# Kernel tuning notes

Measured on AMD Instinct MI355X. Metric: run time of the kernel, lower is better.

Reference implementation:

```python
import jax, jax.numpy as jnp
import numpy as np

D_MODEL = 1024
N_HEADS = 16
D_HEAD = D_MODEL // N_HEADS
WINDOW = 64
SCALE = 1.0 / np.sqrt(D_HEAD)


def setup_inputs() -> dict:
    key = jax.random.key(0)
    k1, k2, k3 = jax.random.split(key, 3)
    B, N = 1, 4096
    x = jax.random.normal(k1, (B, N, D_MODEL), dtype=jnp.float32)
    # xavier-uniform-ish init for weights (scaled normal is fine for a numeric reference)
    w_qkv = jax.random.normal(k2, (3 * D_MODEL, D_MODEL), dtype=jnp.float32) * (1.0 / np.sqrt(D_MODEL))
    b_qkv = jnp.zeros((3 * D_MODEL,), dtype=jnp.float32)
    w_out = jax.random.normal(k3, (D_MODEL, D_MODEL), dtype=jnp.float32) * (1.0 / np.sqrt(D_MODEL))
    b_out = jnp.zeros((D_MODEL,), dtype=jnp.float32)
    return {"x": x, "w_qkv": w_qkv, "b_qkv": b_qkv, "w_out": w_out, "b_out": b_out}


def reference(x, w_qkv, b_qkv, w_out, b_out):
    B, N, D = x.shape
    # QKV projection (torch Linear: x @ W^T + b)
    qkv = x @ w_qkv.T + b_qkv                      # [B, N, 3D]
    qkv = qkv.reshape(B, N, 3, N_HEADS, D_HEAD)
    qkv = jnp.transpose(qkv, (2, 0, 3, 1, 4))       # [3, B, H, N, dh]
    q, k, v = qkv[0], qkv[1], qkv[2]
    # dense scores, masked to causal sliding window (faithful to original)
    scores = jnp.einsum('bhqd,bhkd->bhqk', q, k) * SCALE  # [B, H, N, N]
    qpos = jnp.arange(N)[:, None]
    kpos = jnp.arange(N)[None, :]
    diff = qpos - kpos
    mask = (diff >= 0) & (diff < WINDOW)            # [N, N]
    scores = jnp.where(mask[None, None, :, :], scores, -jnp.inf)
    attn = jax.nn.softmax(scores, axis=-1)          # every query has >=1 valid key (self)
    out = jnp.einsum('bhqk,bhkd->bhqd', attn, v)    # [B, H, N, dh]
    out = jnp.transpose(out, (0, 2, 1, 3)).reshape(B, N, D)
    out = out @ w_out.T + b_out
    return out
```

## Files before the change

kernel.cpp:

```cpp
#include <hip/hip_runtime.h>
#include <hip/hip_bf16.h>
#include <stdint.h>
#include <stddef.h>

#define NSEQ  4096
#define DM    1024
#define NHEAD 16
#define DHEAD 64
#define WIN   64

using short8 = __attribute__((ext_vector_type(8))) short;
using f32x4  = __attribute__((ext_vector_type(4))) float;

#define GLOBAL_AS __attribute__((address_space(1)))
#define LDS_AS    __attribute__((address_space(3)))

__device__ __forceinline__ unsigned short f2bf(float f) {
  union { float f; unsigned int u; } v; v.f = f;
  unsigned int r = v.u + 0x7FFFu + ((v.u >> 16) & 1u);
  return (unsigned short)(r >> 16);
}

__device__ __forceinline__ void gload_lds16(void* lds, const void* g) {
  __builtin_amdgcn_global_load_lds((const GLOBAL_AS unsigned int*)g,
                                   (LDS_AS unsigned int*)lds, 16, 0, 0);
}

#define NX4 1048576
#define NW4 786432
__global__ void cvt_all(const float* __restrict__ x,
                        const float* __restrict__ wqkv,
                        const float* __restrict__ wout,
                        unsigned short* __restrict__ dst) {
  int i = blockIdx.x * blockDim.x + threadIdx.x;
  float4 f;
  if (i < NX4)            f = ((const float4*)x)[i];
  else if (i < NX4 + NW4) f = ((const float4*)wqkv)[i - NX4];
  else                    f = ((const float4*)wout)[i - (NX4 + NW4)];
  ushort4 o;
  o.x = f2bf(f.x); o.y = f2bf(f.y); o.z = f2bf(f.z); o.w = f2bf(f.w);
  ((ushort4*)dst)[i] = o;
}

template<int EPI>
__global__ __launch_bounds__(256)
void gemm3(const unsigned short* __restrict__ A,
           const unsigned short* __restrict__ B,
           const float* __restrict__ bias,
           float* __restrict__ Cf,
           unsigned short* __restrict__ qo,
           unsigned short* __restrict__ ko,
           unsigned short* __restrict__ vo,
           int M, int N, int K) {
  __shared__ short lds[3][8192];

  const int nbn = N >> 7;
  const int bm  = blockIdx.x / nbn;
  const int bn  = blockIdx.x % nbn;
  const int m0  = bm << 7, n0 = bn << 7;
  const int tid = threadIdx.x, w = tid >> 6, l = tid & 63;
  const int wr  = w >> 1, wc = w & 1;
  const int l15 = l & 15, l4 = l >> 4;

  const int skel = ((l & 3) << 3) ^ ((l >= 32) << 4);
  const int roff = l15 * 32 + ((l4 * 8) ^ ((l15 >= 8) * 16));

  f32x4 acc[4][4] = {};
  const int NT = K >> 5;

  auto stage = [&](int t) {
    const int buf = t % 3;
    const int kb  = t << 5;
#pragma unroll
    for (int r = 0; r < 2; ++r) {
      const int c   = r * 4 + w;
      const int row = c * 16 + (l >> 2);
      gload_lds16(&lds[buf][c * 512 + l * 8],
                  A + (size_t)(m0 + row) * K + kb + skel);
      gload_lds16(&lds[buf][4096 + c * 512 + l * 8],
                  B + (size_t)(n0 + row) * K + kb + skel);
    }
  };

  stage(0);
  stage(1);
  asm volatile("s_waitcnt vmcnt(4)" ::: "memory");
  __builtin_amdgcn_s_barrier();

  for (int t = 0; t < NT; ++t) {
    const short* Ab = &lds[t % 3][0];
    const short* Bb = &lds[t % 3][4096];
    short8 af[4], bf[4];
#pragma unroll
    for (int i = 0; i < 4; ++i) {
      af[i] = *(const short8*)&Ab[(wr * 4 + i) * 512 + roff];
      bf[i] = *(const short8*)&Bb[(wc * 4 + i) * 512 + roff];
    }
    if (t + 2 < NT) stage(t + 2);
    if (t + 2 < NT)       asm volatile("s_waitcnt vmcnt(4)" ::: "memory");
    else if (t + 2 == NT) asm volatile("s_waitcnt vmcnt(0)" ::: "memory");
    __builtin_amdgcn_s_barrier();
    __builtin_amdgcn_s_setprio(1);
#pragma unroll
    for (int mi = 0; mi < 4; ++mi)
#pragma unroll
      for (int ni = 0; ni < 4; ++ni)
        acc[mi][ni] = __builtin_amdgcn_mfma_f32_16x16x32_bf16(
            af[mi], bf[ni], acc[mi][ni], 0, 0, 0);
    __builtin_amdgcn_s_setprio(0);
  }

  if (EPI == 0) {
#pragma unroll
    for (int ni = 0; ni < 4; ++ni) {
      const int n  = n0 + wc * 64 + ni * 16 + l15;
      const float bv = bias[n];
      const int region = n >> 10;
#pragma unroll
      for (int mi = 0; mi < 4; ++mi) {
        const int mb = m0 + wr * 64 + mi * 16 + l4 * 4;
        if (region == 0) {
          const int h = (n >> 6) & 15, d = n & 63;
#pragma unroll
          for (int r = 0; r < 4; ++r)
            qo[((size_t)(h * NSEQ + mb + r)) * DHEAD + d] =
                f2bf((acc[mi][ni][r] + bv) * 0.125f);
        } else if (region == 1) {
          const int nn = n - 1024;
          const int h = nn >> 6, d = nn & 63;
#pragma unroll
          for (int r = 0; r < 4; ++r)
            ko[((size_t)(h * NSEQ + mb + r)) * DHEAD + d] =
                f2bf(acc[mi][ni][r] + bv);
        } else {
          const int nn = n - 2048;
          ushort4 pk;
          pk.x = f2bf(acc[mi][ni][0] + bv);
          pk.y = f2bf(acc[mi][ni][1] + bv);
          pk.z = f2bf(acc[mi][ni][2] + bv);
          pk.w = f2bf(acc[mi][ni][3] + bv);
          *(ushort4*)&vo[(size_t)nn * NSEQ + mb] = pk;
        }
      }
    }
  } else {
#pragma unroll
    for (int ni = 0; ni < 4; ++ni) {
      const int n  = n0 + wc * 64 + ni * 16 + l15;
      const float bv = bias[n];
#pragma unroll
      for (int mi = 0; mi < 4; ++mi) {
        const int mb = m0 + wr * 64 + mi * 16 + l4 * 4;
#pragma unroll
        for (int r = 0; r < 4; ++r)
          Cf[(size_t)(mb + r) * N + n] = acc[mi][ni][r] + bv;
      }
    }
  }
}

__global__ __launch_bounds__(256)
void attn_kernel(const unsigned short* __restrict__ Qb,
                 const unsigned short* __restrict__ Kb,
                 const unsigned short* __restrict__ Vt,
                 unsigned short* __restrict__ att) {
  __shared__ short Pl[4][16][136];
  const int h  = blockIdx.x >> 6;
  const int q0 = (blockIdx.x & 63) << 6;
  const int w  = threadIdx.x >> 6;
  const int l  = threadIdx.x & 63;
  const int l15 = l & 15, l4 = l >> 4;
  const int qw = q0 + w * 16;

  const unsigned short* Qh = Qb + (size_t)h * NSEQ * DHEAD;
  const unsigned short* Kh = Kb + (size_t)h * NSEQ * DHEAD;
  const unsigned short* Vh = Vt + (size_t)h * DHEAD * NSEQ;

  short8 aq[2];
  {
    const int qrow = qw + l15;
    aq[0] = *(const short8*)&Qh[(size_t)qrow * DHEAD + l4 * 8];
    aq[1] = *(const short8*)&Qh[(size_t)qrow * DHEAD + 32 + l4 * 8];
  }

  f32x4 s[8] = {};
#pragma unroll
  for (int t = 0; t < 8; ++t) {
    int j  = q0 - 64 + t * 16 + l15;
    int jc = j < 0 ? 0 : j;
    short8 b0 = *(const short8*)&Kh[(size_t)jc * DHEAD + l4 * 8];
    short8 b1 = *(const short8*)&Kh[(size_t)jc * DHEAD + 32 + l4 * 8];
    s[t] = __builtin_amdgcn_mfma_f32_16x16x32_bf16(aq[0], b0, s[t], 0, 0, 0);
    s[t] = __builtin_amdgcn_mfma_f32_16x16x32_bf16(aq[1], b1, s[t], 0, 0, 0);
  }

  float rmax[4] = {-3e38f, -3e38f, -3e38f, -3e38f};
#pragma unroll
  for (int t = 0; t < 8; ++t)
#pragma unroll
    for (int r = 0; r < 4; ++r) {
      const int i = qw + l4 * 4 + r;
      const int j = q0 - 64 + t * 16 + l15;
      const int diff = i - j;
      float sv = (j >= 0 && diff >= 0 && diff < WIN) ? s[t][r] : -3e38f;
      s[t][r] = sv;
      rmax[r] = fmaxf(rmax[r], sv);
    }
#pragma unroll
  for (int r = 0; r < 4; ++r)
#pragma unroll
    for (int m = 1; m < 16; m <<= 1)
      rmax[r] = fmaxf(rmax[r], __shfl_xor(rmax[r], m, 64));

  float rsum[4] = {0.f, 0.f, 0.f, 0.f};
#pragma unroll
  for (int t = 0; t < 8; ++t)
#pragma unroll
    for (int r = 0; r < 4; ++r) {
      float p = __expf(s[t][r] - rmax[r]);
      s[t][r] = p;
      rsum[r] += p;
    }
#pragma unroll
  for (int r = 0; r < 4; ++r)
#pragma unroll
    for (int m = 1; m < 16; m <<= 1)
      rsum[r] += __shfl_xor(rsum[r], m, 64);

#pragma unroll
  for (int t = 0; t < 8; ++t)
#pragma unroll
    for (int r = 0; r < 4; ++r)
      Pl[w][l4 * 4 + r][t * 16 + l15] = (short)f2bf(s[t][r]);

  f32x4 o[4] = {};
#pragma unroll
  for (int ks = 0; ks < 4; ++ks) {
    short8 ap = *(const short8*)&Pl[w][l15][ks * 32 + l4 * 8];
    int jg = q0 - 64 + ks * 32 + l4 * 8;
    if (jg < 0) jg = 0;
#pragma unroll
    for (int dt = 0; dt < 4; ++dt) {
      const int d = dt * 16 + l15;
      short8 bv = *(const short8*)&Vh[(size_t)d * NSEQ + jg];
      o[dt] = __builtin_amdgcn_mfma_f32_16x16x32_bf16(ap, bv, o[dt], 0, 0, 0);
    }
  }

#pragma unroll
  for (int r = 0; r < 4; ++r) {
    const float rinv = 1.0f / rsum[r];
    const int m = qw + l4 * 4 + r;
#pragma unroll
    for (int dt = 0; dt < 4; ++dt)
      att[(size_t)m * DM + h * DHEAD + dt * 16 + l15] = f2bf(o[dt][r] * rinv);
  }
}

extern "C" void kernel_launch(void* const* d_in, const int* in_sizes, int n_in,
                              void* d_out, int out_size, void* d_ws, size_t ws_size,
                              hipStream_t stream) {
  const float* x    = (const float*)d_in[0];
  const float* wqkv = (const float*)d_in[1];
  const float* bqkv = (const float*)d_in[2];
  const float* wout = (const float*)d_in[3];
  const float* bout = (const float*)d_in[4];
  float* out = (float*)d_out;

  unsigned short* ws = (unsigned short*)d_ws;
  unsigned short* xb    = ws;
  unsigned short* wqkvb = xb    + (size_t)NSEQ * DM;
  unsigned short* woutb = wqkvb + (size_t)3 * DM * DM;
  unsigned short* qb    = woutb + (size_t)DM * DM;
  unsigned short* kb    = qb    + (size_t)NSEQ * DM;
  unsigned short* vtb   = kb    + (size_t)NSEQ * DM;
  unsigned short* attb  = vtb   + (size_t)NSEQ * DM;

  cvt_all<<<8192, 256, 0, stream>>>(x, wqkv, wout, xb);

  gemm3<0><<<(NSEQ / 128) * (3 * DM / 128), 256, 0, stream>>>(
      xb, wqkvb, bqkv, nullptr, qb, kb, vtb, NSEQ, 3 * DM, DM);

  attn_kernel<<<NHEAD * (NSEQ / 64), 256, 0, stream>>>(qb, kb, vtb, attb);

  gemm3<1><<<(NSEQ / 128) * (DM / 128), 256, 0, stream>>>(
      attb, woutb, bout, out, nullptr, nullptr, nullptr, NSEQ, DM, DM);
}
```

Measured before the change: 89.58 us.

## Load GEMM B operand directly from global into registers, stage only A in LDS

The GEMM kernel no longer stages the B (weight) tile through LDS. Each wave now reads its B fragments straight from global memory into registers every k-step, and only the A tile goes through the triple-buffered LDS pipeline. This halves LDS use, and the launch bound now asks for 4 blocks per CU to raise occupancy. The cost is that the B global loads are issued just before the MFMAs that use them with no prefetch, so their latency is exposed each iteration. Those loads are also strided 16-byte reads that waves sharing a column tile repeat.

```diff
diff --git a/kernel.cpp b/kernel.cpp
--- a/kernel.cpp
+++ b/kernel.cpp
@@ -43,8 +43,8 @@
 }
 
 template<int EPI>
-__global__ __launch_bounds__(256)
-void gemm3(const unsigned short* __restrict__ A,
+__global__ __launch_bounds__(256, 4)
+void gemm4(const unsigned short* __restrict__ A,
            const unsigned short* __restrict__ B,
            const float* __restrict__ bias,
            float* __restrict__ Cf,
@@ -52,7 +52,7 @@
            unsigned short* __restrict__ ko,
            unsigned short* __restrict__ vo,
            int M, int N, int K) {
-  __shared__ short lds[3][8192];
+  __shared__ short lds[3][4096];
 
   const int nbn = N >> 7;
   const int bm  = blockIdx.x / nbn;
@@ -64,11 +64,12 @@
 
   const int skel = ((l & 3) << 3) ^ ((l >= 32) << 4);
   const int roff = l15 * 32 + ((l4 * 8) ^ ((l15 >= 8) * 16));
+  const unsigned short* Bb = B + (size_t)(n0 + wc * 64 + l15) * K + l4 * 8;
 
   f32x4 acc[4][4] = {};
   const int NT = K >> 5;
 
-  auto stage = [&](int t) {
+  auto stageA = [&](int t) {
     const int buf = t % 3;
     const int kb  = t << 5;
 #pragma unroll
@@ -77,28 +78,29 @@
       const int row = c * 16 + (l >> 2);
       gload_lds16(&lds[buf][c * 512 + l * 8],
                   A + (size_t)(m0 + row) * K + kb + skel);
-      gload_lds16(&lds[buf][4096 + c * 512 + l * 8],
-                  B + (size_t)(n0 + row) * K + kb + skel);
     }
   };
 
-  stage(0);
-  stage(1);
-  asm volatile("s_waitcnt vmcnt(4)" ::: "memory");
+  stageA(0);
+  stageA(1);
+  asm volatile("s_waitcnt vmcnt(2)" ::: "memory");
   __builtin_amdgcn_s_barrier();
 
   for (int t = 0; t < NT; ++t) {
     const short* Ab = &lds[t % 3][0];
-    const short* Bb = &lds[t % 3][4096];
     short8 af[4], bf[4];
 #pragma unroll
-    for (int i = 0; i < 4; ++i) {
+    for (int i = 0; i < 4; ++i)
       af[i] = *(const short8*)&Ab[(wr * 4 + i) * 512 + roff];
-      bf[i] = *(const short8*)&Bb[(wc * 4 + i) * 512 + roff];
-    }
-    if (t + 2 < NT) stage(t + 2);
-    if (t + 2 < NT)       asm volatile("s_waitcnt vmcnt(4)" ::: "memory");
-    else if (t + 2 == NT) asm volatile("s_waitcnt vmcnt(0)" ::: "memory");
+#pragma unroll
+    for (int ni = 0; ni < 4; ++ni)
+      bf[ni] = *(const short8*)&Bb[(size_t)ni * 16 * K + (t << 5)];
+    if (t + 2 < NT) {
+      stageA(t + 2);
+      asm volatile("s_waitcnt vmcnt(6)" ::: "memory");
+    } else {
+      asm volatile("s_waitcnt vmcnt(4)" ::: "memory");
+    }
     __builtin_amdgcn_s_barrier();
     __builtin_amdgcn_s_setprio(1);
 #pragma unroll
@@ -278,11 +280,11 @@
 
   cvt_all<<<8192, 256, 0, stream>>>(x, wqkv, wout, xb);
 
-  gemm3<0><<<(NSEQ / 128) * (3 * DM / 128), 256, 0, stream>>>(
+  gemm4<0><<<(NSEQ / 128) * (3 * DM / 128), 256, 0, stream>>>(
       xb, wqkvb, bqkv, nullptr, qb, kb, vtb, NSEQ, 3 * DM, DM);
 
   attn_kernel<<<NHEAD * (NSEQ / 64), 256, 0, stream>>>(qb, kb, vtb, attb);
 
-  gemm3<1><<<(NSEQ / 128) * (DM / 128), 256, 0, stream>>>(
+  gemm4<1><<<(NSEQ / 128) * (DM / 128), 256, 0, stream>>>(
       attb, woutb, bout, out, nullptr, nullptr, nullptr, NSEQ, DM, DM);
 }
```

Measured after the change: 116.8 us. +30.4%, slower.

## Add dedicated 256x256-tile QKV GEMM kernel with 512 threads and deeper staging

Applied to the files above, without the earlier changes.

Replaces the templated 128x128 QKV projection GEMM with a specialized kernel using 256x256 output tiles, 8 waves, a K-step of 64, and double-buffered 128KB LDS with staggered async loads. The goal is higher data reuse per loaded tile and fewer global loads for the largest GEMM. The trade-off is only 192 blocks at one block per CU, which may underfill the 256 CUs, plus more register pressure from the 8x4 accumulator array. The output-projection GEMM is simplified to a non-templated version.

```diff
diff --git a/kernel.cpp b/kernel.cpp
--- a/kernel.cpp
+++ b/kernel.cpp
@@ -42,15 +42,126 @@
   ((ushort4*)dst)[i] = o;
 }
 
-template<int EPI>
+__global__ __launch_bounds__(512, 1)
+void gemm_qkv(const unsigned short* __restrict__ A,
+              const unsigned short* __restrict__ B,
+              const float* __restrict__ bias,
+              unsigned short* __restrict__ qo,
+              unsigned short* __restrict__ ko,
+              unsigned short* __restrict__ vo) {
+  __shared__ short lds[65536];
+
+  const int bm = blockIdx.x / 12;
+  const int bn = blockIdx.x % 12;
+  const int m0 = bm << 8, n0 = bn << 8;
+  const int tid = threadIdx.x, w = tid >> 6, l = tid & 63;
+  const int wr = w >> 2, wc = w & 3;
+  const int l15 = l & 15, l4 = l >> 4;
+  const int srow = l >> 2;
+  const int skel = ((l & 3) << 3) ^ ((l >= 32) << 4);
+  const int roff = l15 * 32 + ((l4 * 8) ^ ((l15 >= 8) * 16));
+
+  f32x4 acc[8][4] = {};
+
+  auto stageA = [&](int j, int qm) {
+    const int base = (j & 1) * 32768 + qm * 8192;
+#pragma unroll
+    for (int r = 0; r < 2; ++r) {
+      const int c = r * 8 + w;
+      gload_lds16(&lds[base + c * 512 + l * 8],
+                  A + (size_t)(m0 + qm * 128 + (c >> 1) * 16 + srow) * 1024
+                    + (j << 6) + (c & 1) * 32 + skel);
+    }
+  };
+  auto stageB = [&](int j, int qk) {
+    const int base = (j & 1) * 32768 + 16384 + qk * 8192;
+#pragma unroll
+    for (int r = 0; r < 2; ++r) {
+      const int c = r * 8 + w;
+      gload_lds16(&lds[base + c * 512 + l * 8],
+                  B + (size_t)(n0 + c * 16 + srow) * 1024
+                    + (j << 6) + qk * 32 + skel);
+    }
+  };
+
+  stageA(0, 0); stageA(0, 1); stageB(0, 1); stageB(0, 0); stageB(1, 0);
+  asm volatile("s_waitcnt vmcnt(2)" ::: "memory");
+  __builtin_amdgcn_s_barrier();
+
+  const int NT = 16;
+  for (int j = 0; j < NT; ++j) {
+    const int buf = (j & 1) * 32768;
+    const short* Ah = &lds[buf + wr * 8192];
+#pragma unroll
+    for (int p = 0; p < 4; ++p) {
+      const int qm = p & 1, qk = p >> 1;
+      const short* Bh = &lds[buf + 16384 + qk * 8192];
+      short8 af[4], bf[4];
+#pragma unroll
+      for (int i = 0; i < 4; ++i)
+        af[i] = *(const short8*)&Ah[(qm * 4 + i) * 1024 + qk * 512 + roff];
+#pragma unroll
+      for (int i = 0; i < 4; ++i)
+        bf[i] = *(const short8*)&Bh[(wc * 4 + i) * 512 + roff];
+      if (p == 0 && j + 1 < NT) { stageA(j + 1, 0); stageA(j + 1, 1); stageB(j + 1, 1); }
+      if (p == 2 && j + 2 < NT) { stageB(j + 2, 0); }
+      if (p == 3) {
+        if (j + 2 < NT) asm volatile("s_waitcnt vmcnt(2)" ::: "memory");
+        else            asm volatile("s_waitcnt vmcnt(0)" ::: "memory");
+      } else {
+        asm volatile("" ::: "memory");
+      }
+      __builtin_amdgcn_s_barrier();
+      __builtin_amdgcn_s_setprio(1);
+#pragma unroll
+      for (int i = 0; i < 4; ++i)
+#pragma unroll
+        for (int ni = 0; ni < 4; ++ni)
+          acc[qm * 4 + i][ni] = __builtin_amdgcn_mfma_f32_16x16x32_bf16(
+              af[i], bf[ni], acc[qm * 4 + i][ni], 0, 0, 0);
+      __builtin_amdgcn_s_setprio(0);
+    }
+  }
+
+#pragma unroll
+  for (int ni = 0; ni < 4; ++ni) {
+    const int n  = n0 + wc * 64 + ni * 16 + l15;
+    const float bv = bias[n];
+    const int region = n >> 10;
+#pragma unroll
+    for (int mi = 0; mi < 8; ++mi) {
+      const int mb = m0 + wr * 128 + mi * 16 + l4 * 4;
+      if (region == 0) {
+        const int h = (n >> 6) & 15, d = n & 63;
+#pragma unroll
+        for (int r = 0; r < 4; ++r)
+          qo[((size_t)(h * NSEQ + mb + r)) * DHEAD + d] =
+              f2bf((acc[mi][ni][r] + bv) * 0.125f);
+      } else if (region == 1) {
+        const int nn = n - 1024;
+        const int h = nn >> 6, d = nn & 63;
+#pragma unroll
+        for (int r = 0; r < 4; ++r)
+          ko[((size_t)(h * NSEQ + mb + r)) * DHEAD + d] =
+              f2bf(acc[mi][ni][r] + bv);
+      } else {
+        const int nn = n - 2048;
+        ushort4 pk;
+        pk.x = f2bf(acc[mi][ni][0] + bv);
+        pk.y = f2bf(acc[mi][ni][1] + bv);
+        pk.z = f2bf(acc[mi][ni][2] + bv);
+        pk.w = f2bf(acc[mi][ni][3] + bv);
+        *(ushort4*)&vo[(size_t)nn * NSEQ + mb] = pk;
+      }
+    }
+  }
+}
+
 __global__ __launch_bounds__(256)
 void gemm3(const unsigned short* __restrict__ A,
            const unsigned short* __restrict__ B,
            const float* __restrict__ bias,
            float* __restrict__ Cf,
-           unsigned short* __restrict__ qo,
-           unsigned short* __restrict__ ko,
-           unsigned short* __restrict__ vo,
            int M, int N, int K) {
   __shared__ short lds[3][8192];
 
@@ -110,51 +221,16 @@
     __builtin_amdgcn_s_setprio(0);
   }
 
-  if (EPI == 0) {
-#pragma unroll
-    for (int ni = 0; ni < 4; ++ni) {
-      const int n  = n0 + wc * 64 + ni * 16 + l15;
-      const float bv = bias[n];
-      const int region = n >> 10;
-#pragma unroll
-      for (int mi = 0; mi < 4; ++mi) {
-        const int mb = m0 + wr * 64 + mi * 16 + l4 * 4;
-        if (region == 0) {
-          const int h = (n >> 6) & 15, d = n & 63;
-#pragma unroll
-          for (int r = 0; r < 4; ++r)
-            qo[((size_t)(h * NSEQ + mb + r)) * DHEAD + d] =
-                f2bf((acc[mi][ni][r] + bv) * 0.125f);
-        } else if (region == 1) {
-          const int nn = n - 1024;
-          const int h = nn >> 6, d = nn & 63;
-#pragma unroll
-          for (int r = 0; r < 4; ++r)
-            ko[((size_t)(h * NSEQ + mb + r)) * DHEAD + d] =
-                f2bf(acc[mi][ni][r] + bv);
-        } else {
-          const int nn = n - 2048;
-          ushort4 pk;
-          pk.x = f2bf(acc[mi][ni][0] + bv);
-          pk.y = f2bf(acc[mi][ni][1] + bv);
-          pk.z = f2bf(acc[mi][ni][2] + bv);
-          pk.w = f2bf(acc[mi][ni][3] + bv);
-          *(ushort4*)&vo[(size_t)nn * NSEQ + mb] = pk;
-        }
-      }
-    }
-  } else {
-#pragma unroll
-    for (int ni = 0; ni < 4; ++ni) {
-      const int n  = n0 + wc * 64 + ni * 16 + l15;
-      const float bv = bias[n];
-#pragma unroll
-      for (int mi = 0; mi < 4; ++mi) {
-        const int mb = m0 + wr * 64 + mi * 16 + l4 * 4;
-#pragma unroll
-        for (int r = 0; r < 4; ++r)
-          Cf[(size_t)(mb + r) * N + n] = acc[mi][ni][r] + bv;
-      }
+#pragma unroll
+  for (int ni = 0; ni < 4; ++ni) {
+    const int n  = n0 + wc * 64 + ni * 16 + l15;
+    const float bv = bias[n];
+#pragma unroll
+    for (int mi = 0; mi < 4; ++mi) {
+      const int mb = m0 + wr * 64 + mi * 16 + l4 * 4;
+#pragma unroll
+      for (int r = 0; r < 4; ++r)
+        Cf[(size_t)(mb + r) * N + n] = acc[mi][ni][r] + bv;
     }
   }
 }
@@ -278,11 +354,11 @@
 
   cvt_all<<<8192, 256, 0, stream>>>(x, wqkv, wout, xb);
 
-  gemm3<0><<<(NSEQ / 128) * (3 * DM / 128), 256, 0, stream>>>(
-      xb, wqkvb, bqkv, nullptr, qb, kb, vtb, NSEQ, 3 * DM, DM);
+  gemm_qkv<<<(NSEQ / 256) * (3 * DM / 256), 512, 0, stream>>>(
+      xb, wqkvb, bqkv, qb, kb, vtb);
 
   attn_kernel<<<NHEAD * (NSEQ / 64), 256, 0, stream>>>(qb, kb, vtb, attb);
 
-  gemm3<1><<<(NSEQ / 128) * (DM / 128), 256, 0, stream>>>(
-      attb, woutb, bout, out, nullptr, nullptr, nullptr, NSEQ, DM, DM);
-}
+  gemm3<<<(NSEQ / 128) * (DM / 128), 256, 0, stream>>>(
+      attb, woutb, bout, out, NSEQ, DM, DM);
+}
```

After: 88.29 us. No clear change (-1.4%).
